# Kernel tuning notes

Measured on AMD Instinct MI355X. Metric: run time of the kernel, lower is better.

Reference implementation:

```python
import jax, jax.numpy as jnp
import numpy as np

B, S, MAX_K, MID, V = 4, 512, 32, 32, 32000


def _lin(x, W, b):
    # torch nn.Linear convention: W is [out, in]
    return x @ W.T + b


def _label_count_segment(vals):
    """Distinct-label counts over prefixes [0:1],[0:2],...,[0:K] of the kNN labels."""
    Bv, Sv, K = vals.shape
    mask = jnp.triu(jnp.ones((K, K), dtype=bool), k=1)  # [K,K], True above diagonal
    # row i of expand keeps labels [0:i+1], rest filled with -1 (as in masked_fill)
    ev = jnp.where(mask, jnp.array(-1, vals.dtype), vals[:, :, None, :])  # [B,S,K,K]
    s = jnp.sort(ev, axis=-1)
    # zero-out adjacent duplicates (keep first occurrence)
    dedup = jnp.concatenate([s[..., :1], s[..., 1:] * (s[..., 1:] != s[..., :-1])], axis=-1)
    cnt = (dedup != 0).sum(-1)  # [B,S,K]
    cnt = cnt.at[..., :-1].add(-1)  # remove the single surviving -1 for rows 0..K-2
    return cnt


def setup_inputs():
    key = jax.random.key(0)
    ks = jax.random.split(key, 16)
    tgt_index = jax.random.randint(ks[0], (B, S, MAX_K), 0, V)
    knn_dists = jax.random.uniform(ks[1], (B, S, MAX_K), jnp.float32, 1e-3, 10.0)
    knn_key_feature = jax.random.uniform(ks[2], (B, S, MAX_K), jnp.float32, 1e-4, 1.0)
    network_probs = jax.random.uniform(ks[3], (B, S, V), jnp.float32, 1e-6, 1.0)
    network_probs = network_probs / network_probs.sum(-1, keepdims=True)
    network_select_probs = jax.random.uniform(ks[4], (B, S, MAX_K), jnp.float32, 1e-6, 1e-2)
    init = lambda k, shape: 0.02 * jax.random.normal(k, shape, jnp.float32)
    return {
        "tgt_index": tgt_index,
        "knn_dists": knn_dists,
        "knn_key_feature": knn_key_feature,
        "network_probs": network_probs,
        "network_select_probs": network_select_probs,
        # distance_func: Linear(2K+8, 1)
        "W_func": init(ks[5], (1, 2 * MAX_K + 8)), "b_func": init(ks[6], (1,)),
        # distance_fc1: Linear(2,4) -> Tanh -> Linear(4,1)
        "W1a": init(ks[7], (4, 2)), "b1a": init(ks[8], (4,)),
        "W1b": init(ks[9], (1, 4)), "b1b": init(ks[10], (1,)),
        # distance_fc2: Linear(2K, mid) -> Tanh -> Linear(mid, 2)
        "W2a": init(ks[11], (MID, 2 * MAX_K)), "b2a": init(ks[12], (MID,)),
        "W2b": init(ks[13], (2, MID)), "b2b": init(ks[14], (2,)),
    }


def reference(tgt_index, knn_dists, knn_key_feature, network_probs, network_select_probs,
              W_func, b_func, W1a, b1a, W1b, b1b, W2a, b2a, W2b, b2b):
    Bv, Sv, K = knn_dists.shape
    Vv = network_probs.shape[-1]
    label_counts = _label_count_segment(tgt_index)  # [B,S,K] int
    log_key = jnp.log(knn_key_feature)
    log_sel = jnp.log(network_select_probs)
    all_key_feature = jnp.stack([log_key, log_sel], axis=-1)  # [B,S,K,2]
    top_prob, _ = jax.lax.top_k(network_probs, 8)  # [B,S,8]
    knn_feat = jnp.concatenate([knn_dists, label_counts.astype(knn_dists.dtype)], -1)  # [B,S,2K]
    noise_logit = _lin(jnp.tanh(_lin(all_key_feature, W1a, b1a)), W1b, b1b).squeeze(-1)  # [B,S,K]
    sim_in = jnp.concatenate([jnp.log(top_prob), log_key, log_sel], -1)  # [B,S,2K+8]
    sim_lambda = _lin(sim_in, W_func, b_func)  # [B,S,1]
    lambda_logit = _lin(jnp.tanh(_lin(knn_feat, W2a, b2a)), W2b, b2b)  # [B,S,2]
    knn_lambda = jax.nn.softmax(jnp.concatenate([lambda_logit[..., :1], sim_lambda], -1), -1)[..., :1]
    tempe = jax.nn.sigmoid(lambda_logit[..., 1:2])  # [B,S,1]
    probs = jax.nn.softmax(-knn_dists * tempe + noise_logit, -1)  # [B,S,K]
    bi = jnp.arange(Bv)[:, None, None]
    si = jnp.arange(Sv)[None, :, None]
    knn_prob = jnp.zeros((Bv, Sv, Vv), probs.dtype).at[bi, si, tgt_index].set(probs)
    return knn_prob, knn_lambda
```

## Files before the change

### kernel.cpp

```cpp
#include <hip/hip_runtime.h>

typedef unsigned long long ull;
typedef float f4 __attribute__((ext_vector_type(4)));

#define TOKENS 2048
#define KNN    32
#define VOCAB  32000

#define INSF(vv) do {                                                        \
    float x_ = (vv);                                                         \
    if (x_ > t7) {                                                           \
        float h_;                                                            \
        h_ = fmaxf(t0, x_); x_ = fminf(t0, x_); t0 = h_;                     \
        h_ = fmaxf(t1, x_); x_ = fminf(t1, x_); t1 = h_;                     \
        h_ = fmaxf(t2, x_); x_ = fminf(t2, x_); t2 = h_;                     \
        h_ = fmaxf(t3, x_); x_ = fminf(t3, x_); t3 = h_;                     \
        h_ = fmaxf(t4, x_); x_ = fminf(t4, x_); t4 = h_;                     \
        h_ = fmaxf(t5, x_); x_ = fminf(t5, x_); t5 = h_;                     \
        h_ = fmaxf(t6, x_); x_ = fminf(t6, x_); t6 = h_;                     \
        t7 = fmaxf(t7, x_);                                                  \
    }                                                                        \
} while (0)

#define PROC(i) do {                                                         \
    f4 v_ = np4[(i)];                                                        \
    o4[(i)] = z4;                                                            \
    float m_ = fmaxf(fmaxf(v_.x, v_.y), fmaxf(v_.z, v_.w));                  \
    if (m_ > t7) {                                                           \
        INSF(v_.x); INSF(v_.y); INSF(v_.z); INSF(v_.w);                      \
    }                                                                        \
} while (0)

#define INSK(key) do {                                                       \
    ull k_ = (key);                                                          \
    if (k_ > c7) {                                                           \
        ull tmp_;                                                            \
        if (k_ > c0) { tmp_ = c0; c0 = k_; k_ = tmp_; }                      \
        if (k_ > c1) { tmp_ = c1; c1 = k_; k_ = tmp_; }                      \
        if (k_ > c2) { tmp_ = c2; c2 = k_; k_ = tmp_; }                      \
        if (k_ > c3) { tmp_ = c3; c3 = k_; k_ = tmp_; }                      \
        if (k_ > c4) { tmp_ = c4; c4 = k_; k_ = tmp_; }                      \
        if (k_ > c5) { tmp_ = c5; c5 = k_; k_ = tmp_; }                      \
        if (k_ > c6) { tmp_ = c6; c6 = k_; k_ = tmp_; }                      \
        c7 = (k_ > c7) ? k_ : c7;                                            \
    }                                                                        \
} while (0)

__global__ __launch_bounds__(256, 8)
void rc_kernel(const int*   __restrict__ tgt_index,
               const float* __restrict__ knn_dists,
               const float* __restrict__ knn_key,
               const float* __restrict__ net_probs,
               const float* __restrict__ net_sel,
               const float* __restrict__ W_func, const float* __restrict__ b_func,
               const float* __restrict__ W1a,    const float* __restrict__ b1a,
               const float* __restrict__ W1b,    const float* __restrict__ b1b,
               const float* __restrict__ W2a,    const float* __restrict__ b2a,
               const float* __restrict__ W2b,    const float* __restrict__ b2b,
               float* __restrict__ out)
{
    const int t   = blockIdx.x;
    const int tid = threadIdx.x;

    __shared__ float s_cand[256 * 8];
    __shared__ int   s_tgt[KNN];
    __shared__ float s_dist[KNN];
    __shared__ float s_cnt[KNN];
    __shared__ float s_top8[8];

    int   tg = 0;
    float d = 0.f, lk = 0.f, ls = 0.f;
    if (tid < KNN) {
        tg = tgt_index[t * KNN + tid];
        d  = knn_dists[t * KNN + tid];
        lk = logf(knn_key[t * KNN + tid]);
        ls = logf(net_sel[t * KNN + tid]);
        s_tgt[tid]  = tg;
        s_dist[tid] = d;
    }

    float t0 = 0.f, t1 = 0.f, t2 = 0.f, t3 = 0.f,
          t4 = 0.f, t5 = 0.f, t6 = 0.f, t7 = 0.f;
    const f4* np4 = (const f4*)(net_probs + (size_t)t * VOCAB);
    f4*       o4  = (f4*)(out + (size_t)t * VOCAB);
    const f4  z4  = (f4){0.f, 0.f, 0.f, 0.f};
    #pragma unroll 2
    for (int k = 0; k < 31; ++k) {
        PROC(tid + (k << 8));
    }
    if (tid < 64) {
        PROC(tid + (31 << 8));
    }

    s_cand[tid * 8 + 0] = t0;  s_cand[tid * 8 + 1] = t1;
    s_cand[tid * 8 + 2] = t2;  s_cand[tid * 8 + 3] = t3;
    s_cand[tid * 8 + 4] = t4;  s_cand[tid * 8 + 5] = t5;
    s_cand[tid * 8 + 6] = t6;  s_cand[tid * 8 + 7] = t7;
    __syncthreads();

    if (tid < 64) {
        ull c0 = 0, c1 = 0, c2 = 0, c3 = 0, c4 = 0, c5 = 0, c6 = 0, c7 = 0;
        for (int k = 0; k < 32; ++k) {
            int idx = tid + (k << 6);
            ull key = (((ull)__float_as_uint(s_cand[idx])) << 32) | (unsigned)idx;
            INSK(key);
        }
        for (int r = 0; r < 8; ++r) {
            ull g = c0;
            #pragma unroll
            for (int off = 1; off < 64; off <<= 1) {
                ull o = __shfl_xor(g, off);
                if (o > g) g = o;
            }
            if (c0 == g) {
                c0 = c1; c1 = c2; c2 = c3; c3 = c4; c4 = c5; c5 = c6; c6 = c7; c7 = 0;
            }
            if (tid == 0) s_top8[r] = __uint_as_float((unsigned)(g >> 32));
        }
    }
    __syncthreads();

    if (tid < KNN) {
        int fo = (tg != 0) ? 1 : 0;
        if (fo) {
            for (int j = 0; j < tid; ++j)
                if (s_tgt[j] == tg) { fo = 0; break; }
        }
        int c = fo;
        #pragma unroll
        for (int off = 1; off < KNN; off <<= 1) {
            int n = __shfl_up(c, off, KNN);
            if (tid >= off) c += n;
        }
        s_cnt[tid] = (float)c;
    }
    __syncthreads();

    if (tid < KNN) {
        float noise = b1b[0];
        #pragma unroll
        for (int j = 0; j < 4; ++j) {
            float z = tanhf(W1a[2 * j] * lk + W1a[2 * j + 1] * ls + b1a[j]);
            noise += W1b[j] * z;
        }

        float sp = W_func[8 + tid] * lk + W_func[40 + tid] * ls;
        if (tid < 8) sp += W_func[tid] * logf(s_top8[tid]);
        #pragma unroll
        for (int off = 16; off; off >>= 1) sp += __shfl_xor(sp, off, KNN);
        float sim = sp + b_func[0];

        float h = b2a[tid];
        const float* wr = W2a + tid * 64;
        #pragma unroll 8
        for (int i = 0; i < KNN; ++i) h += wr[i] * s_dist[i];
        #pragma unroll 8
        for (int i = 0; i < KNN; ++i) h += wr[KNN + i] * s_cnt[i];
        h = tanhf(h);
        float p0 = W2b[tid] * h;
        float p1 = W2b[KNN + tid] * h;
        #pragma unroll
        for (int off = 16; off; off >>= 1) {
            p0 += __shfl_xor(p0, off, KNN);
            p1 += __shfl_xor(p1, off, KNN);
        }
        float l0 = p0 + b2b[0];
        float l1 = p1 + b2b[1];

        float tempe = 1.f / (1.f + expf(-l1));
        float lam   = 1.f / (1.f + expf(-(l0 - sim)));

        float logit = -d * tempe + noise;
        float mx = logit;
        #pragma unroll
        for (int off = 16; off; off >>= 1) mx = fmaxf(mx, __shfl_xor(mx, off, KNN));
        float e = expf(logit - mx);
        float se = e;
        #pragma unroll
        for (int off = 16; off; off >>= 1) se += __shfl_xor(se, off, KNN);
        float p = e / se;

        bool wrte = true;
        for (int j = tid + 1; j < KNN; ++j)
            if (s_tgt[j] == tg) { wrte = false; break; }
        if (wrte) out[(size_t)t * VOCAB + tg] = p;

        if (tid == 0) out[(size_t)TOKENS * VOCAB + t] = lam;
    }
}

extern "C" void kernel_launch(void* const* d_in, const int* in_sizes, int n_in,
                              void* d_out, int out_size, void* d_ws, size_t ws_size,
                              hipStream_t stream) {
    rc_kernel<<<TOKENS, 256, 0, stream>>>(
        (const int*)  d_in[0],
        (const float*)d_in[1],
        (const float*)d_in[2],
        (const float*)d_in[3],
        (const float*)d_in[4],
        (const float*)d_in[5],  (const float*)d_in[6],
        (const float*)d_in[7],  (const float*)d_in[8],
        (const float*)d_in[9],  (const float*)d_in[10],
        (const float*)d_in[11], (const float*)d_in[12],
        (const float*)d_in[13], (const float*)d_in[14],
        (float*)d_out);
}
```

Measured before the change: 138.4 us.

## Replace per-thread top-8 insertion with threshold filter and candidate compaction

```diff
diff --git a/kernel.cpp b/kernel.cpp
--- a/kernel.cpp
+++ b/kernel.cpp
@@ -6,6 +6,22 @@
 #define TOKENS 2048
 #define KNN    32
 #define VOCAB  32000
+#define CAP    2048
+
+#define INSK(key) do {                                                       \
+    ull k_ = (key);                                                          \
+    if (k_ > c7) {                                                           \
+        ull tmp_;                                                            \
+        if (k_ > c0) { tmp_ = c0; c0 = k_; k_ = tmp_; }                      \
+        if (k_ > c1) { tmp_ = c1; c1 = k_; k_ = tmp_; }                      \
+        if (k_ > c2) { tmp_ = c2; c2 = k_; k_ = tmp_; }                      \
+        if (k_ > c3) { tmp_ = c3; c3 = k_; k_ = tmp_; }                      \
+        if (k_ > c4) { tmp_ = c4; c4 = k_; k_ = tmp_; }                      \
+        if (k_ > c5) { tmp_ = c5; c5 = k_; k_ = tmp_; }                      \
+        if (k_ > c6) { tmp_ = c6; c6 = k_; k_ = tmp_; }                      \
+        c7 = (k_ > c7) ? k_ : c7;                                            \
+    }                                                                        \
+} while (0)
 
 #define INSF(vv) do {                                                        \
     float x_ = (vv);                                                         \
@@ -22,29 +38,7 @@
     }                                                                        \
 } while (0)
 
-#define PROC(i) do {                                                         \
-    f4 v_ = np4[(i)];                                                        \
-    o4[(i)] = z4;                                                            \
-    float m_ = fmaxf(fmaxf(v_.x, v_.y), fmaxf(v_.z, v_.w));                  \
-    if (m_ > t7) {                                                           \
-        INSF(v_.x); INSF(v_.y); INSF(v_.z); INSF(v_.w);                      \
-    }                                                                        \
-} while (0)
-
-#define INSK(key) do {                                                       \
-    ull k_ = (key);                                                          \
-    if (k_ > c7) {                                                           \
-        ull tmp_;                                                            \
-        if (k_ > c0) { tmp_ = c0; c0 = k_; k_ = tmp_; }                      \
-        if (k_ > c1) { tmp_ = c1; c1 = k_; k_ = tmp_; }                      \
-        if (k_ > c2) { tmp_ = c2; c2 = k_; k_ = tmp_; }                      \
-        if (k_ > c3) { tmp_ = c3; c3 = k_; k_ = tmp_; }                      \
-        if (k_ > c4) { tmp_ = c4; c4 = k_; k_ = tmp_; }                      \
-        if (k_ > c5) { tmp_ = c5; c5 = k_; k_ = tmp_; }                      \
-        if (k_ > c6) { tmp_ = c6; c6 = k_; k_ = tmp_; }                      \
-        c7 = (k_ > c7) ? k_ : c7;                                            \
-    }                                                                        \
-} while (0)
+#define MAX4(v_) fmaxf(fmaxf(v_.x, v_.y), fmaxf(v_.z, v_.w))
 
 __global__ __launch_bounds__(256, 8)
 void rc_kernel(const int*   __restrict__ tgt_index,
@@ -62,11 +56,16 @@
     const int t   = blockIdx.x;
     const int tid = threadIdx.x;
 
-    __shared__ float s_cand[256 * 8];
+    __shared__ float s_max[256];
+    __shared__ float s_cand[CAP];
+    __shared__ int   s_ncand;
+    __shared__ float s_thr;
     __shared__ int   s_tgt[KNN];
     __shared__ float s_dist[KNN];
     __shared__ float s_cnt[KNN];
     __shared__ float s_top8[8];
+
+    if (tid == 0) s_ncand = 0;
 
     int   tg = 0;
     float d = 0.f, lk = 0.f, ls = 0.f;
@@ -79,34 +78,36 @@
         s_dist[tid] = d;
     }
 
-    float t0 = 0.f, t1 = 0.f, t2 = 0.f, t3 = 0.f,
-          t4 = 0.f, t5 = 0.f, t6 = 0.f, t7 = 0.f;
     const f4* np4 = (const f4*)(net_probs + (size_t)t * VOCAB);
     f4*       o4  = (f4*)(out + (size_t)t * VOCAB);
     const f4  z4  = (f4){0.f, 0.f, 0.f, 0.f};
-    #pragma unroll 2
+
+    float m = 0.f;
+    #pragma unroll
     for (int k = 0; k < 31; ++k) {
-        PROC(tid + (k << 8));
+        f4 v = np4[tid + (k << 8)];
+        o4[tid + (k << 8)] = z4;
+        m = fmaxf(m, MAX4(v));
     }
     if (tid < 64) {
-        PROC(tid + (31 << 8));
-    }
-
-    s_cand[tid * 8 + 0] = t0;  s_cand[tid * 8 + 1] = t1;
-    s_cand[tid * 8 + 2] = t2;  s_cand[tid * 8 + 3] = t3;
-    s_cand[tid * 8 + 4] = t4;  s_cand[tid * 8 + 5] = t5;
-    s_cand[tid * 8 + 6] = t6;  s_cand[tid * 8 + 7] = t7;
+        f4 v = np4[tid + (31 << 8)];
+        o4[tid + (31 << 8)] = z4;
+        m = fmaxf(m, MAX4(v));
+    }
+    s_max[tid] = m;
     __syncthreads();
 
     if (tid < 64) {
         ull c0 = 0, c1 = 0, c2 = 0, c3 = 0, c4 = 0, c5 = 0, c6 = 0, c7 = 0;
-        for (int k = 0; k < 32; ++k) {
+        #pragma unroll
+        for (int k = 0; k < 4; ++k) {
             int idx = tid + (k << 6);
-            ull key = (((ull)__float_as_uint(s_cand[idx])) << 32) | (unsigned)idx;
+            ull key = (((ull)__float_as_uint(s_max[idx])) << 32) | (unsigned)idx;
             INSK(key);
         }
+        ull g = 0;
         for (int r = 0; r < 8; ++r) {
-            ull g = c0;
+            g = c0;
             #pragma unroll
             for (int off = 1; off < 64; off <<= 1) {
                 ull o = __shfl_xor(g, off);
@@ -115,7 +116,92 @@
             if (c0 == g) {
                 c0 = c1; c1 = c2; c2 = c3; c3 = c4; c4 = c5; c5 = c6; c6 = c7; c7 = 0;
             }
-            if (tid == 0) s_top8[r] = __uint_as_float((unsigned)(g >> 32));
+        }
+        if (tid == 0) s_thr = __uint_as_float((unsigned)(g >> 32));
+    }
+    __syncthreads();
+    const float T = s_thr;
+
+    #pragma unroll 4
+    for (int k = 0; k < 31; ++k) {
+        f4 v = np4[tid + (k << 8)];
+        if (MAX4(v) >= T) {
+            if (v.x >= T) { int p = atomicAdd(&s_ncand, 1); if (p < CAP) s_cand[p] = v.x; }
+            if (v.y >= T) { int p = atomicAdd(&s_ncand, 1); if (p < CAP) s_cand[p] = v.y; }
+            if (v.z >= T) { int p = atomicAdd(&s_ncand, 1); if (p < CAP) s_cand[p] = v.z; }
+            if (v.w >= T) { int p = atomicAdd(&s_ncand, 1); if (p < CAP) s_cand[p] = v.w; }
+        }
+    }
+    if (tid < 64) {
+        f4 v = np4[tid + (31 << 8)];
+        if (MAX4(v) >= T) {
+            if (v.x >= T) { int p = atomicAdd(&s_ncand, 1); if (p < CAP) s_cand[p] = v.x; }
+            if (v.y >= T) { int p = atomicAdd(&s_ncand, 1); if (p < CAP) s_cand[p] = v.y; }
+            if (v.z >= T) { int p = atomicAdd(&s_ncand, 1); if (p < CAP) s_cand[p] = v.z; }
+            if (v.w >= T) { int p = atomicAdd(&s_ncand, 1); if (p < CAP) s_cand[p] = v.w; }
+        }
+    }
+    __syncthreads();
+    const int n = s_ncand;
+
+    if (n <= CAP) {
+        if (tid < 64) {
+            ull c0 = 0, c1 = 0, c2 = 0, c3 = 0, c4 = 0, c5 = 0, c6 = 0, c7 = 0;
+            for (int i = tid; i < n; i += 64) {
+                ull key = (((ull)__float_as_uint(s_cand[i])) << 32) | (unsigned)i;
+                INSK(key);
+            }
+            for (int r = 0; r < 8; ++r) {
+                ull g = c0;
+                #pragma unroll
+                for (int off = 1; off < 64; off <<= 1) {
+                    ull o = __shfl_xor(g, off);
+                    if (o > g) g = o;
+                }
+                if (c0 == g && g != 0ULL) {
+                    c0 = c1; c1 = c2; c2 = c3; c3 = c4; c4 = c5; c5 = c6; c6 = c7; c7 = 0;
+                }
+                if (tid == 0) s_top8[r] = __uint_as_float((unsigned)(g >> 32));
+            }
+        }
+    } else {
+        float t0 = 0.f, t1 = 0.f, t2 = 0.f, t3 = 0.f,
+              t4 = 0.f, t5 = 0.f, t6 = 0.f, t7 = 0.f;
+        for (int k = 0; k < 31; ++k) {
+            f4 v = np4[tid + (k << 8)];
+            float mm = MAX4(v);
+            if (mm > t7) { INSF(v.x); INSF(v.y); INSF(v.z); INSF(v.w); }
+        }
+        if (tid < 64) {
+            f4 v = np4[tid + (31 << 8)];
+            float mm = MAX4(v);
+            if (mm > t7) { INSF(v.x); INSF(v.y); INSF(v.z); INSF(v.w); }
+        }
+        __syncthreads();
+        s_cand[tid * 8 + 0] = t0;  s_cand[tid * 8 + 1] = t1;
+        s_cand[tid * 8 + 2] = t2;  s_cand[tid * 8 + 3] = t3;
+        s_cand[tid * 8 + 4] = t4;  s_cand[tid * 8 + 5] = t5;
+        s_cand[tid * 8 + 6] = t6;  s_cand[tid * 8 + 7] = t7;
+        __syncthreads();
+        if (tid < 64) {
+            ull c0 = 0, c1 = 0, c2 = 0, c3 = 0, c4 = 0, c5 = 0, c6 = 0, c7 = 0;
+            for (int k = 0; k < 32; ++k) {
+                int idx = tid + (k << 6);
+                ull key = (((ull)__float_as_uint(s_cand[idx])) << 32) | (unsigned)idx;
+                INSK(key);
+            }
+            for (int r = 0; r < 8; ++r) {
+                ull g = c0;
+                #pragma unroll
+                for (int off = 1; off < 64; off <<= 1) {
+                    ull o = __shfl_xor(g, off);
+                    if (o > g) g = o;
+                }
+                if (c0 == g) {
+                    c0 = c1; c1 = c2; c2 = c3; c3 = c4; c4 = c5; c5 = c6; c6 = c7; c7 = 0;
+                }
+                if (tid == 0) s_top8[r] = __uint_as_float((unsigned)(g >> 32));
+            }
         }
     }
     __syncthreads();
@@ -129,8 +215,8 @@
         int c = fo;
         #pragma unroll
         for (int off = 1; off < KNN; off <<= 1) {
-            int n = __shfl_up(c, off, KNN);
-            if (tid >= off) c += n;
+            int n2 = __shfl_up(c, off, KNN);
+            if (tid >= off) c += n2;
         }
         s_cnt[tid] = (float)c;
     }
```

Measured after the change: 170.4 us. 23.1% more time.
